# Optimization experiments

Hardware: AMD Instinct MI355X
Metric: run time of the kernel (lower is better)

Reference implementation:

```python
import jax, jax.numpy as jnp
import numpy as np

N = 100000   # nodes
E = 1600000  # edges (avg degree 16)
D = 64       # in_dim == hidden_dim
L = 3        # num_layers
EPS = 1e-5   # LayerNorm eps


def setup_inputs() -> dict:
    key = jax.random.key(0)
    k0, k1, k2 = jax.random.split(key, 3)
    x = jax.random.normal(k0, (N, D), dtype=jnp.float32)
    edge_index = jax.random.randint(k1, (2, E), 0, N, dtype=jnp.int32)
    # Per-layer GCN weights/bias (Glorot-ish scale) and LayerNorm params
    Ws = jax.random.normal(k2, (L, D, D), dtype=jnp.float32) / np.float32(np.sqrt(D))
    bs = jnp.zeros((L, D), dtype=jnp.float32)
    gammas = jnp.ones((L, D), dtype=jnp.float32)
    betas = jnp.zeros((L, D), dtype=jnp.float32)
    return {"x": x, "Ws": Ws, "bs": bs, "gammas": gammas, "betas": betas,
            "edge_index": edge_index}


def _layer_norm(h, gamma, beta):
    mu = jnp.mean(h, axis=-1, keepdims=True)
    var = jnp.mean(jnp.square(h - mu), axis=-1, keepdims=True)
    return (h - mu) * jax.lax.rsqrt(var + EPS) * gamma + beta


def reference(x, Ws, bs, gammas, betas, edge_index):
    # GCNConv semantics: add self-loops, symmetric deg^{-1/2} normalization.
    loop = jnp.arange(N, dtype=edge_index.dtype)
    row = jnp.concatenate([edge_index[0], loop])  # source (gather)
    col = jnp.concatenate([edge_index[1], loop])  # target (scatter)
    deg = jax.ops.segment_sum(jnp.ones_like(col, dtype=x.dtype), col, num_segments=N)
    dinv = jnp.where(deg > 0, jax.lax.rsqrt(deg), jnp.zeros_like(deg))
    enorm = dinv[row] * dinv[col]  # (E+N,)

    h = x
    for i in range(L):
        hw = h @ Ws[i]                                   # (N, D) small GEMM
        msg = hw[row] * enorm[:, None]                   # (E+N, D) gather
        h = jax.ops.segment_sum(msg, col, num_segments=N) + bs[i]  # scatter-add
        h = _layer_norm(h, gammas[i], betas[i])
        if i < L - 1:
            h = jax.nn.relu(h)                           # dropout is identity in eval
    return h
```

## Files before the change

### kernel.cpp

```cpp
#include <hip/hip_runtime.h>
#include <hip/hip_bf16.h>


#define DDIM 64
#define EPSV 1e-5f
#define BSHIFT 9
#define BNODES (1 << BSHIFT)
#define NBUCK 256
#define CHUNK 4096

typedef __hip_bfloat16 bf16;
typedef unsigned int u32;
typedef unsigned short u16;
typedef unsigned long long u64;
typedef __attribute__((ext_vector_type(8))) short frag8;
typedef __attribute__((ext_vector_type(4))) float f32x4;

__device__ __forceinline__ float b2f(bf16 v) { return __bfloat162float(v); }
__device__ __forceinline__ float bits2f(u16 b) {
    union { u32 u; float f; } c; c.u = ((u32)b) << 16; return c.f;
}
__device__ __forceinline__ float lo2f(u32 u) {
    union { u32 x; float f; } c; c.x = u << 16; return c.f;
}
__device__ __forceinline__ float hi2f(u32 u) {
    union { u32 x; float f; } c; c.x = u & 0xffff0000u; return c.f;
}
__device__ __forceinline__ u32 packbf(float a, float b) {
    union { bf16 h; u16 u; } ca, cb;
    ca.h = __float2bfloat16(a);
    cb.h = __float2bfloat16(b);
    return (u32)ca.u | ((u32)cb.u << 16);
}
__device__ __forceinline__ float cvt_load(const void* src, int i, int f32) {
    return f32 ? ((const float*)src)[i] : b2f(((const bf16*)src)[i]);
}

__global__ void detect_dtype(const u32* __restrict__ g, int* __restrict__ flagF32) {
    if (threadIdx.x == 0 && blockIdx.x == 0) *flagF32 = (g[0] == 0x3F800000u) ? 1 : 0;
}

__global__ void convert_x(const void* __restrict__ src, bf16* __restrict__ dst,
                          const int* __restrict__ flagF32,
                          const float* __restrict__ dinv, int n) {
    int i = blockIdx.x * blockDim.x + threadIdx.x;
    if (i >= n) return;
    dst[i] = __float2bfloat16(cvt_load(src, i, *flagF32) * dinv[i >> 6]);
}

__global__ void convert_params(const void* __restrict__ W, const void* __restrict__ b,
                               const void* __restrict__ g, const void* __restrict__ bt,
                               bf16* __restrict__ dWt, bf16* __restrict__ db,
                               bf16* __restrict__ dg, bf16* __restrict__ dbt,
                               const int* __restrict__ flagF32, int nW, int nS) {
    int i = blockIdx.x * blockDim.x + threadIdx.x;
    int f = *flagF32;
    if (i < nW) {
        int L = i >> 12, n = (i >> 6) & 63, k = i & 63;
        dWt[i] = __float2bfloat16(cvt_load(W, (L << 12) | (k << 6) | n, f));
        return;
    }
    i -= nW;
    if (i < nS) { db[i] = __float2bfloat16(cvt_load(b, i, f)); return; }
    i -= nS;
    if (i < nS) { dg[i] = __float2bfloat16(cvt_load(g, i, f)); return; }
    i -= nS;
    if (i < nS) { dbt[i] = __float2bfloat16(cvt_load(bt, i, f)); }
}


__global__ void __launch_bounds__(256) bucket_count(const int* __restrict__ col,
                                                    int* __restrict__ bcnt, int E) {
    __shared__ int h[NBUCK];
    int tid = threadIdx.x;
    h[tid] = 0;
    __syncthreads();
    for (int i = blockIdx.x * blockDim.x + tid; i < E; i += gridDim.x * blockDim.x)
        atomicAdd(&h[col[i] >> BSHIFT], 1);
    __syncthreads();
    int v = h[tid];
    if (v) atomicAdd(&bcnt[tid], v);
}

__global__ void bucket_scan(const int* __restrict__ bcnt, int* __restrict__ bbase,
                            int* __restrict__ gcur, int nbuck, int E) {
    __shared__ int s[NBUCK];
    int tid = threadIdx.x;
    int v = (tid < nbuck) ? bcnt[tid] : 0;
    s[tid] = v;
    __syncthreads();
    for (int off = 1; off < NBUCK; off <<= 1) {
        int t = (tid >= off) ? s[tid - off] : 0;
        __syncthreads();
        s[tid] += t;
        __syncthreads();
    }
    int excl = s[tid] - v;
    if (tid < nbuck) { bbase[tid] = excl; gcur[tid] = excl; }
    if (tid == 0) bbase[nbuck] = E;
}

__global__ void __launch_bounds__(256) partition_edges(const int* __restrict__ row,
                                                       const int* __restrict__ col,
                                                       int* __restrict__ gcur,
                                                       u64* __restrict__ pairs, int E) {
    __shared__ int hist[NBUCK];
    __shared__ int lbase[NBUCK];
    __shared__ int gdelta[NBUCK];
    __shared__ int lcur[NBUCK];
    __shared__ int sbuf[NBUCK];
    __shared__ int dest[CHUNK];
    __shared__ u64 stage[CHUNK];
    int tid = threadIdx.x;
    int chunk0 = blockIdx.x * CHUNK;
    hist[tid] = 0;
    lcur[tid] = 0;
    __syncthreads();
    int r[16], c[16];
#pragma unroll
    for (int i = 0; i < 16; i++) {
        int idx = chunk0 + i * 256 + tid;
        if (idx < E) {
            r[i] = row[idx];
            c[i] = col[idx];
            atomicAdd(&hist[c[i] >> BSHIFT], 1);
        }
    }
    __syncthreads();
    int h = hist[tid];
    sbuf[tid] = h;
    __syncthreads();
    for (int off = 1; off < 256; off <<= 1) {
        int t = (tid >= off) ? sbuf[tid - off] : 0;
        __syncthreads();
        sbuf[tid] += t;
        __syncthreads();
    }
    int excl = sbuf[tid] - h;
    lbase[tid] = excl;
    int gb = (h > 0) ? atomicAdd(&gcur[tid], h) : 0;
    gdelta[tid] = gb - excl;
    __syncthreads();
#pragma unroll
    for (int i = 0; i < 16; i++) {
        int idx = chunk0 + i * 256 + tid;
        if (idx < E) {
            int b = c[i] >> BSHIFT;
            int pos = lbase[b] + atomicAdd(&lcur[b], 1);
            stage[pos] = ((u64)(u32)c[i] << 32) | (u32)r[i];
            dest[pos] = gdelta[b];
        }
    }
    __syncthreads();
    int chunkN = min(CHUNK, E - chunk0);
    for (int j = tid; j < chunkN; j += 256)
        pairs[(size_t)(dest[j] + j)] = stage[j];
}

__global__ void __launch_bounds__(512) build_csr(const u64* __restrict__ pairs,
                                                 const int* __restrict__ bbase,
                                                 int* __restrict__ ptr,
                                                 int* __restrict__ srcs,
                                                 float* __restrict__ dinv,
                                                 int N, int E) {
    __shared__ int deg[BNODES];
    __shared__ int lptr[BNODES];
    __shared__ int lfill[BNODES];
    int b = blockIdx.x;
    int node0 = b << BSHIFT;
    int nn = min(BNODES, N - node0);
    int tid = threadIdx.x;
    deg[tid] = 0;
    lfill[tid] = 0;
    __syncthreads();
    int beg = bbase[b], end = bbase[b + 1];
    for (int i = beg + tid; i < end; i += 512)
        atomicAdd(&deg[(int)(pairs[i] >> 32) - node0], 1);
    __syncthreads();
    int d = deg[tid];
    lptr[tid] = d;
    __syncthreads();
    for (int off = 1; off < BNODES; off <<= 1) {
        int t = (tid >= off) ? lptr[tid - off] : 0;
        __syncthreads();
        lptr[tid] += t;
        __syncthreads();
    }
    int excl = lptr[tid] - d;
    lptr[tid] = beg + excl;
    if (tid < nn) {
        ptr[node0 + tid] = beg + excl;
        dinv[node0 + tid] = rsqrtf((float)(d + 1));
    }
    if (b == 0 && tid == 0) ptr[N] = E;
    __syncthreads();
    for (int i = beg + tid; i < end; i += 512) {
        u64 pr = pairs[i];
        int li = (int)(pr >> 32) - node0;
        int p = lptr[li] + atomicAdd(&lfill[li], 1);
        srcs[p] = (int)(pr & 0xffffffffu);
    }
}


__global__ void __launch_bounds__(256) aggregate(const bf16* __restrict__ Hs,
                                                 const int* __restrict__ ptr,
                                                 const int* __restrict__ srcs,
                                                 const float* __restrict__ dinv,
                                                 bf16* __restrict__ AG, int N) {
    int t = blockIdx.x * blockDim.x + threadIdx.x;
    int w = t >> 6;
    int lane = t & 63;
    int half = lane >> 5;
    int lane32 = lane & 31;
    int v = w * 2 + half;
    if (v >= N) return;
    int sub = lane32 >> 3;
    int quad = lane & 7;
    uint4 selfq = ((const uint4*)(Hs + ((size_t)v << 6)))[quad];
    int beg = ptr[v], end = ptr[v + 1];
    float a0 = 0.f, a1 = 0.f, a2 = 0.f, a3 = 0.f;
    float a4 = 0.f, a5 = 0.f, a6 = 0.f, a7 = 0.f;
    for (int base = beg; base < end; base += 32) {
        int rem = end - base;
        int m = rem < 32 ? rem : 32;
        int sidx = (lane32 < m) ? srcs[base + lane32] : 0;
        for (int j = 0; j < m; j += 8) {
            int e0 = j + sub;
            int e1 = j + 4 + sub;
            int s0 = __shfl(sidx, (half << 5) + e0, 64);
            int s1 = __shfl(sidx, (half << 5) + e1, 64);
            float k0 = (e0 < m) ? 1.f : 0.f;
            float k1 = (e1 < m) ? 1.f : 0.f;
            uint4 q0 = ((const uint4*)(Hs + ((size_t)s0 << 6)))[quad];
            uint4 q1 = ((const uint4*)(Hs + ((size_t)s1 << 6)))[quad];
            a0 = fmaf(lo2f(q0.x), k0, a0); a1 = fmaf(hi2f(q0.x), k0, a1);
            a2 = fmaf(lo2f(q0.y), k0, a2); a3 = fmaf(hi2f(q0.y), k0, a3);
            a4 = fmaf(lo2f(q0.z), k0, a4); a5 = fmaf(hi2f(q0.z), k0, a5);
            a6 = fmaf(lo2f(q0.w), k0, a6); a7 = fmaf(hi2f(q0.w), k0, a7);
            a0 = fmaf(lo2f(q1.x), k1, a0); a1 = fmaf(hi2f(q1.x), k1, a1);
            a2 = fmaf(lo2f(q1.y), k1, a2); a3 = fmaf(hi2f(q1.y), k1, a3);
            a4 = fmaf(lo2f(q1.z), k1, a4); a5 = fmaf(hi2f(q1.z), k1, a5);
            a6 = fmaf(lo2f(q1.w), k1, a6); a7 = fmaf(hi2f(q1.w), k1, a7);
        }
    }
#pragma unroll
    for (int d = 8; d < 32; d <<= 1) {
        a0 += __shfl_xor(a0, d, 64); a1 += __shfl_xor(a1, d, 64);
        a2 += __shfl_xor(a2, d, 64); a3 += __shfl_xor(a3, d, 64);
        a4 += __shfl_xor(a4, d, 64); a5 += __shfl_xor(a5, d, 64);
        a6 += __shfl_xor(a6, d, 64); a7 += __shfl_xor(a7, d, 64);
    }
    if (sub == 0) {
        a0 += lo2f(selfq.x); a1 += hi2f(selfq.x);
        a2 += lo2f(selfq.y); a3 += hi2f(selfq.y);
        a4 += lo2f(selfq.z); a5 += hi2f(selfq.z);
        a6 += lo2f(selfq.w); a7 += hi2f(selfq.w);
        float dv = dinv[v];
        uint4 o;
        o.x = packbf(a0 * dv, a1 * dv);
        o.y = packbf(a2 * dv, a3 * dv);
        o.z = packbf(a4 * dv, a5 * dv);
        o.w = packbf(a6 * dv, a7 * dv);
        ((uint4*)(AG + ((size_t)v << 6)))[quad] = o;
    }
}


__global__ void __launch_bounds__(256, 4) gemm_ln(const bf16* __restrict__ AG,
                                                  const bf16* __restrict__ Wt,
                                                  const bf16* __restrict__ bias,
                                                  const bf16* __restrict__ gamma,
                                                  const bf16* __restrict__ beta,
                                                  bf16* __restrict__ outB,
                                                  float* __restrict__ outF,
                                                  const int* __restrict__ flagF32,
                                                  const float* __restrict__ dscale,
                                                  int relu, int last, int N) {
    int tid = threadIdx.x;
    int wv = tid >> 6, lane = tid & 63;
    int n = lane & 15, q = lane >> 4;
    int r0 = blockIdx.x * 64 + wv * 16;

    int arow = r0 + n;
    int arowc = arow < N ? arow : N - 1;
    const uint4* ap = (const uint4*)(AG + ((size_t)arowc << 6));
    frag8 af0 = __builtin_bit_cast(frag8, ap[q]);
    frag8 af1 = __builtin_bit_cast(frag8, ap[4 + q]);

    f32x4 acc[4];
#pragma unroll
    for (int t = 0; t < 4; t++) acc[t] = (f32x4){0.f, 0.f, 0.f, 0.f};
#pragma unroll
    for (int t = 0; t < 4; t++) {
        const uint4* bp = (const uint4*)(Wt + (((size_t)(t * 16 + n)) << 6));
        frag8 bf0 = __builtin_bit_cast(frag8, bp[q]);
        frag8 bf1 = __builtin_bit_cast(frag8, bp[4 + q]);
        acc[t] = __builtin_amdgcn_mfma_f32_16x16x32_bf16(af0, bf0, acc[t], 0, 0, 0);
        acc[t] = __builtin_amdgcn_mfma_f32_16x16x32_bf16(af1, bf1, acc[t], 0, 0, 0);
    }

    float bb[4], gg[4], be[4];
#pragma unroll
    for (int t = 0; t < 4; t++) {
        int c = t * 16 + n;
        bb[t] = b2f(bias[c]);
        gg[t] = b2f(gamma[c]);
        be[t] = b2f(beta[c]);
    }
    int f32o = last ? flagF32[0] : 0;

#pragma unroll
    for (int r = 0; r < 4; r++) {
        int rr = r0 + q * 4 + r;
        float v0 = acc[0][r] + bb[0];
        float v1 = acc[1][r] + bb[1];
        float v2 = acc[2][r] + bb[2];
        float v3 = acc[3][r] + bb[3];
        float s = v0 + v1 + v2 + v3;
        s += __shfl_xor(s, 1, 64);
        s += __shfl_xor(s, 2, 64);
        s += __shfl_xor(s, 4, 64);
        s += __shfl_xor(s, 8, 64);
        float mu = s * (1.f / 64.f);
        float d0 = v0 - mu, d1 = v1 - mu, d2 = v2 - mu, d3 = v3 - mu;
        float sq = d0 * d0 + d1 * d1 + d2 * d2 + d3 * d3;
        sq += __shfl_xor(sq, 1, 64);
        sq += __shfl_xor(sq, 2, 64);
        sq += __shfl_xor(sq, 4, 64);
        sq += __shfl_xor(sq, 8, 64);
        float rs = rsqrtf(sq * (1.f / 64.f) + EPSV);
        float o0 = d0 * rs * gg[0] + be[0];
        float o1 = d1 * rs * gg[1] + be[1];
        float o2 = d2 * rs * gg[2] + be[2];
        float o3 = d3 * rs * gg[3] + be[3];
        if (relu) {
            o0 = fmaxf(o0, 0.f); o1 = fmaxf(o1, 0.f);
            o2 = fmaxf(o2, 0.f); o3 = fmaxf(o3, 0.f);
        }
        if (rr < N) {
            if (dscale) {
                float sc = dscale[rr];
                o0 *= sc; o1 *= sc; o2 *= sc; o3 *= sc;
            }
            size_t base = ((size_t)rr << 6) + n;
            if (f32o) {
                outF[base] = o0; outF[base + 16] = o1;
                outF[base + 32] = o2; outF[base + 48] = o3;
            } else {
                outB[base] = __float2bfloat16(o0);
                outB[base + 16] = __float2bfloat16(o1);
                outB[base + 32] = __float2bfloat16(o2);
                outB[base + 48] = __float2bfloat16(o3);
            }
        }
    }
}


extern "C" void kernel_launch(void* const* d_in, const int* in_sizes, int n_in,
                              void* d_out, int out_size, void* d_ws, size_t ws_size,
                              hipStream_t stream) {
    (void)n_in; (void)out_size; (void)ws_size;
    const void* x      = d_in[0];
    const void* Wsrc   = d_in[1];
    const void* bsrc   = d_in[2];
    const void* gsrc   = d_in[3];
    const void* btsrc  = d_in[4];
    const int*  ei     = (const int*)d_in[5];
    int N = in_sizes[0] / DDIM;
    int E = in_sizes[5] / 2;
    const int* rowp = ei;
    const int* colp = ei + E;

    char* w = (char*)d_ws;
    auto alloc = [&](size_t bytes) -> char* {
        char* p = w;
        w += (bytes + 255) / 256 * 256;
        return p;
    };
    int*   flag  = (int*)alloc(4);
    int*   gcur  = (int*)alloc(NBUCK * 4);
    int*   bcnt  = (int*)alloc(NBUCK * 4);
    int*   bbase = (int*)alloc((NBUCK + 1) * 4);
    int*   ptr   = (int*)alloc((size_t)(N + 1) * 4);
    int*   srcs  = (int*)alloc((size_t)E * 4);
    float* dinv  = (float*)alloc((size_t)N * 4);
    char*  hreg  = alloc((size_t)N * DDIM * 2);
    bf16*  H     = (bf16*)hreg;
    u64*   pairs = (u64*)hreg;
    bf16*  wsW   = (bf16*)alloc((size_t)3 * 4096 * 2);
    bf16*  wsB   = (bf16*)alloc(192 * 2);
    bf16*  wsG   = (bf16*)alloc(192 * 2);
    bf16*  wsBt  = (bf16*)alloc(192 * 2);
    bf16*  AG    = (bf16*)alloc((size_t)N * DDIM * 2);

    const int tb = 256;
    int nbuck = (N + BNODES - 1) >> BSHIFT;
    detect_dtype<<<1, 64, 0, stream>>>((const u32*)gsrc, flag);
    hipMemsetAsync(bcnt, 0, NBUCK * 4, stream);
    bucket_count<<<256, tb, 0, stream>>>(colp, bcnt, E);
    bucket_scan<<<1, NBUCK, 0, stream>>>(bcnt, bbase, gcur, nbuck, E);
    partition_edges<<<(E + CHUNK - 1) / CHUNK, tb, 0, stream>>>(rowp, colp, gcur, pairs, E);
    build_csr<<<nbuck, 512, 0, stream>>>(pairs, bbase, ptr, srcs, dinv, N, E);

    convert_x<<<(N * DDIM + tb - 1) / tb, tb, 0, stream>>>(x, H, flag, dinv, N * DDIM);
    int nPar = 3 * 4096 + 3 * 192;
    convert_params<<<(nPar + tb - 1) / tb, tb, 0, stream>>>(Wsrc, bsrc, gsrc, btsrc,
                                                            wsW, wsB, wsG, wsBt,
                                                            flag, 3 * 4096, 192);

    int aggBlocks = (N * 32 + tb - 1) / tb;
    int gBlocks = (N + 63) / 64;

    aggregate<<<aggBlocks, tb, 0, stream>>>(H, ptr, srcs, dinv, AG, N);
    gemm_ln<<<gBlocks, tb, 0, stream>>>(AG, wsW + 0 * 4096, wsB + 0,   wsG + 0,   wsBt + 0,
                                        H, nullptr, flag, dinv, 1, 0, N);
    aggregate<<<aggBlocks, tb, 0, stream>>>(H, ptr, srcs, dinv, AG, N);
    gemm_ln<<<gBlocks, tb, 0, stream>>>(AG, wsW + 1 * 4096, wsB + 64,  wsG + 64,  wsBt + 64,
                                        H, nullptr, flag, dinv, 1, 0, N);
    aggregate<<<aggBlocks, tb, 0, stream>>>(H, ptr, srcs, dinv, AG, N);
    gemm_ln<<<gBlocks, tb, 0, stream>>>(AG, wsW + 2 * 4096, wsB + 128, wsG + 128, wsBt + 128,
                                        (bf16*)d_out, (float*)d_out, flag, nullptr, 0, 1, N);
}
```

Before: 290.9 us.

## Fuse aggregation with GEMM+LayerNorm and merge setup kernels

Merges the per-layer aggregate kernel into the GEMM+LayerNorm kernel. Each wave aggregates its 16 rows into LDS, then feeds the MFMA directly, which removes the intermediate AG round-trip through global memory and one launch per layer. H is now ping-ponged between two buffers because the layer output can no longer overwrite its input. The setup also drops kernels: dtype detection moves into bucket_count, per-block partial histograms replace global atomics and the memset, and the x and parameter conversions become one kernel. The cost is less gather parallelism per wave (8 serial iterations per wave), which may expose gather latency under the raised occupancy hint.

```diff
diff --git a/kernel.cpp b/kernel.cpp
--- a/kernel.cpp
+++ b/kernel.cpp
@@ -8,6 +8,7 @@
 #define BNODES (1 << BSHIFT)
 #define NBUCK 256
 #define CHUNK 4096
+#define CBLKS 256
 
 typedef __hip_bfloat16 bf16;
 typedef unsigned int u32;
@@ -17,9 +18,6 @@
 typedef __attribute__((ext_vector_type(4))) float f32x4;
 
 __device__ __forceinline__ float b2f(bf16 v) { return __bfloat162float(v); }
-__device__ __forceinline__ float bits2f(u16 b) {
-    union { u32 u; float f; } c; c.u = ((u32)b) << 16; return c.f;
-}
 __device__ __forceinline__ float lo2f(u32 u) {
     union { u32 x; float f; } c; c.x = u << 16; return c.f;
 }
@@ -36,57 +34,28 @@
     return f32 ? ((const float*)src)[i] : b2f(((const bf16*)src)[i]);
 }
 
-__global__ void detect_dtype(const u32* __restrict__ g, int* __restrict__ flagF32) {
-    if (threadIdx.x == 0 && blockIdx.x == 0) *flagF32 = (g[0] == 0x3F800000u) ? 1 : 0;
-}
-
-__global__ void convert_x(const void* __restrict__ src, bf16* __restrict__ dst,
-                          const int* __restrict__ flagF32,
-                          const float* __restrict__ dinv, int n) {
-    int i = blockIdx.x * blockDim.x + threadIdx.x;
-    if (i >= n) return;
-    dst[i] = __float2bfloat16(cvt_load(src, i, *flagF32) * dinv[i >> 6]);
-}
-
-__global__ void convert_params(const void* __restrict__ W, const void* __restrict__ b,
-                               const void* __restrict__ g, const void* __restrict__ bt,
-                               bf16* __restrict__ dWt, bf16* __restrict__ db,
-                               bf16* __restrict__ dg, bf16* __restrict__ dbt,
-                               const int* __restrict__ flagF32, int nW, int nS) {
-    int i = blockIdx.x * blockDim.x + threadIdx.x;
-    int f = *flagF32;
-    if (i < nW) {
-        int L = i >> 12, n = (i >> 6) & 63, k = i & 63;
-        dWt[i] = __float2bfloat16(cvt_load(W, (L << 12) | (k << 6) | n, f));
-        return;
-    }
-    i -= nW;
-    if (i < nS) { db[i] = __float2bfloat16(cvt_load(b, i, f)); return; }
-    i -= nS;
-    if (i < nS) { dg[i] = __float2bfloat16(cvt_load(g, i, f)); return; }
-    i -= nS;
-    if (i < nS) { dbt[i] = __float2bfloat16(cvt_load(bt, i, f)); }
-}
-
 
 __global__ void __launch_bounds__(256) bucket_count(const int* __restrict__ col,
-                                                    int* __restrict__ bcnt, int E) {
+                                                    int* __restrict__ partials,
+                                                    const u32* __restrict__ g,
+                                                    int* __restrict__ flagF32, int E) {
     __shared__ int h[NBUCK];
     int tid = threadIdx.x;
+    if (blockIdx.x == 0 && tid == 0) *flagF32 = (g[0] == 0x3F800000u) ? 1 : 0;
     h[tid] = 0;
     __syncthreads();
     for (int i = blockIdx.x * blockDim.x + tid; i < E; i += gridDim.x * blockDim.x)
         atomicAdd(&h[col[i] >> BSHIFT], 1);
     __syncthreads();
-    int v = h[tid];
-    if (v) atomicAdd(&bcnt[tid], v);
-}
-
-__global__ void bucket_scan(const int* __restrict__ bcnt, int* __restrict__ bbase,
+    partials[blockIdx.x * NBUCK + tid] = h[tid];
+}
+
+__global__ void bucket_scan(const int* __restrict__ partials, int* __restrict__ bbase,
                             int* __restrict__ gcur, int nbuck, int E) {
     __shared__ int s[NBUCK];
     int tid = threadIdx.x;
-    int v = (tid < nbuck) ? bcnt[tid] : 0;
+    int v = 0;
+    for (int b = 0; b < CBLKS; b++) v += partials[b * NBUCK + tid];
     s[tid] = v;
     __syncthreads();
     for (int off = 1; off < NBUCK; off <<= 1) {
@@ -202,91 +171,108 @@
     }
 }
 
-
-__global__ void __launch_bounds__(256) aggregate(const bf16* __restrict__ Hs,
-                                                 const int* __restrict__ ptr,
-                                                 const int* __restrict__ srcs,
-                                                 const float* __restrict__ dinv,
-                                                 bf16* __restrict__ AG, int N) {
-    int t = blockIdx.x * blockDim.x + threadIdx.x;
-    int w = t >> 6;
-    int lane = t & 63;
-    int half = lane >> 5;
-    int lane32 = lane & 31;
-    int v = w * 2 + half;
-    if (v >= N) return;
-    int sub = lane32 >> 3;
-    int quad = lane & 7;
-    uint4 selfq = ((const uint4*)(Hs + ((size_t)v << 6)))[quad];
-    int beg = ptr[v], end = ptr[v + 1];
-    float a0 = 0.f, a1 = 0.f, a2 = 0.f, a3 = 0.f;
-    float a4 = 0.f, a5 = 0.f, a6 = 0.f, a7 = 0.f;
-    for (int base = beg; base < end; base += 32) {
-        int rem = end - base;
-        int m = rem < 32 ? rem : 32;
-        int sidx = (lane32 < m) ? srcs[base + lane32] : 0;
-        for (int j = 0; j < m; j += 8) {
-            int e0 = j + sub;
-            int e1 = j + 4 + sub;
-            int s0 = __shfl(sidx, (half << 5) + e0, 64);
-            int s1 = __shfl(sidx, (half << 5) + e1, 64);
-            float k0 = (e0 < m) ? 1.f : 0.f;
-            float k1 = (e1 < m) ? 1.f : 0.f;
-            uint4 q0 = ((const uint4*)(Hs + ((size_t)s0 << 6)))[quad];
-            uint4 q1 = ((const uint4*)(Hs + ((size_t)s1 << 6)))[quad];
-            a0 = fmaf(lo2f(q0.x), k0, a0); a1 = fmaf(hi2f(q0.x), k0, a1);
-            a2 = fmaf(lo2f(q0.y), k0, a2); a3 = fmaf(hi2f(q0.y), k0, a3);
-            a4 = fmaf(lo2f(q0.z), k0, a4); a5 = fmaf(hi2f(q0.z), k0, a5);
-            a6 = fmaf(lo2f(q0.w), k0, a6); a7 = fmaf(hi2f(q0.w), k0, a7);
-            a0 = fmaf(lo2f(q1.x), k1, a0); a1 = fmaf(hi2f(q1.x), k1, a1);
-            a2 = fmaf(lo2f(q1.y), k1, a2); a3 = fmaf(hi2f(q1.y), k1, a3);
-            a4 = fmaf(lo2f(q1.z), k1, a4); a5 = fmaf(hi2f(q1.z), k1, a5);
-            a6 = fmaf(lo2f(q1.w), k1, a6); a7 = fmaf(hi2f(q1.w), k1, a7);
-        }
-    }
-#pragma unroll
-    for (int d = 8; d < 32; d <<= 1) {
-        a0 += __shfl_xor(a0, d, 64); a1 += __shfl_xor(a1, d, 64);
-        a2 += __shfl_xor(a2, d, 64); a3 += __shfl_xor(a3, d, 64);
-        a4 += __shfl_xor(a4, d, 64); a5 += __shfl_xor(a5, d, 64);
-        a6 += __shfl_xor(a6, d, 64); a7 += __shfl_xor(a7, d, 64);
-    }
-    if (sub == 0) {
-        a0 += lo2f(selfq.x); a1 += hi2f(selfq.x);
-        a2 += lo2f(selfq.y); a3 += hi2f(selfq.y);
-        a4 += lo2f(selfq.z); a5 += hi2f(selfq.z);
-        a6 += lo2f(selfq.w); a7 += hi2f(selfq.w);
-        float dv = dinv[v];
-        uint4 o;
-        o.x = packbf(a0 * dv, a1 * dv);
-        o.y = packbf(a2 * dv, a3 * dv);
-        o.z = packbf(a4 * dv, a5 * dv);
-        o.w = packbf(a6 * dv, a7 * dv);
-        ((uint4*)(AG + ((size_t)v << 6)))[quad] = o;
-    }
-}
-
-
-__global__ void __launch_bounds__(256, 4) gemm_ln(const bf16* __restrict__ AG,
-                                                  const bf16* __restrict__ Wt,
-                                                  const bf16* __restrict__ bias,
-                                                  const bf16* __restrict__ gamma,
-                                                  const bf16* __restrict__ beta,
-                                                  bf16* __restrict__ outB,
-                                                  float* __restrict__ outF,
-                                                  const int* __restrict__ flagF32,
-                                                  const float* __restrict__ dscale,
-                                                  int relu, int last, int N) {
+__global__ void convert_all(const void* __restrict__ x, const void* __restrict__ W,
+                            const void* __restrict__ b, const void* __restrict__ g,
+                            const void* __restrict__ bt,
+                            bf16* __restrict__ H, bf16* __restrict__ dWt,
+                            bf16* __restrict__ db, bf16* __restrict__ dg,
+                            bf16* __restrict__ dbt,
+                            const int* __restrict__ flagF32,
+                            const float* __restrict__ dinv, int nX, int nW, int nS) {
+    int i = blockIdx.x * blockDim.x + threadIdx.x;
+    int f = *flagF32;
+    if (i < nX) { H[i] = __float2bfloat16(cvt_load(x, i, f) * dinv[i >> 6]); return; }
+    i -= nX;
+    if (i < nW) {
+        int L = i >> 12, n = (i >> 6) & 63, k = i & 63;
+        dWt[i] = __float2bfloat16(cvt_load(W, (L << 12) | (k << 6) | n, f));
+        return;
+    }
+    i -= nW;
+    if (i < nS) { db[i] = __float2bfloat16(cvt_load(b, i, f)); return; }
+    i -= nS;
+    if (i < nS) { dg[i] = __float2bfloat16(cvt_load(g, i, f)); return; }
+    i -= nS;
+    if (i < nS) { dbt[i] = __float2bfloat16(cvt_load(bt, i, f)); }
+}
+
+
+__global__ void __launch_bounds__(256, 5) fused_layer(const bf16* __restrict__ Hs,
+                                                      const int* __restrict__ ptr,
+                                                      const int* __restrict__ srcs,
+                                                      const float* __restrict__ dinv,
+                                                      const bf16* __restrict__ Wt,
+                                                      const bf16* __restrict__ bias,
+                                                      const bf16* __restrict__ gamma,
+                                                      const bf16* __restrict__ beta,
+                                                      bf16* __restrict__ outB,
+                                                      float* __restrict__ outF,
+                                                      const int* __restrict__ flagF32,
+                                                      const float* __restrict__ dscale,
+                                                      int relu, int last, int N) {
+    __shared__ __align__(16) bf16 lsA[4][16][64];
     int tid = threadIdx.x;
     int wv = tid >> 6, lane = tid & 63;
+    int half = lane >> 5, lane32 = lane & 31;
+    int sub = lane32 >> 3, quad = lane & 7;
+    int r0 = blockIdx.x * 64 + wv * 16;
+
+    for (int it = 0; it < 8; it++) {
+        int v = r0 + it * 2 + half;
+        int vc = v < N ? v : N - 1;
+        uint4 selfq = ((const uint4*)(Hs + ((size_t)vc << 6)))[quad];
+        int beg = 0, end = 0;
+        if (v < N) { beg = ptr[v]; end = ptr[v + 1]; }
+        float a0 = 0.f, a1 = 0.f, a2 = 0.f, a3 = 0.f;
+        float a4 = 0.f, a5 = 0.f, a6 = 0.f, a7 = 0.f;
+        for (int base = beg; base < end; base += 32) {
+            int rem = end - base;
+            int m = rem < 32 ? rem : 32;
+            int sidx = (lane32 < m) ? srcs[base + lane32] : 0;
+            for (int j = 0; j < m; j += 8) {
+                int e0 = j + sub;
+                int e1 = j + 4 + sub;
+                int s0 = __shfl(sidx, (half << 5) + e0, 64);
+                int s1 = __shfl(sidx, (half << 5) + e1, 64);
+                float k0 = (e0 < m) ? 1.f : 0.f;
+                float k1 = (e1 < m) ? 1.f : 0.f;
+                uint4 q0 = ((const uint4*)(Hs + ((size_t)s0 << 6)))[quad];
+                uint4 q1 = ((const uint4*)(Hs + ((size_t)s1 << 6)))[quad];
+                a0 = fmaf(lo2f(q0.x), k0, a0); a1 = fmaf(hi2f(q0.x), k0, a1);
+                a2 = fmaf(lo2f(q0.y), k0, a2); a3 = fmaf(hi2f(q0.y), k0, a3);
+                a4 = fmaf(lo2f(q0.z), k0, a4); a5 = fmaf(hi2f(q0.z), k0, a5);
+                a6 = fmaf(lo2f(q0.w), k0, a6); a7 = fmaf(hi2f(q0.w), k0, a7);
+                a0 = fmaf(lo2f(q1.x), k1, a0); a1 = fmaf(hi2f(q1.x), k1, a1);
+                a2 = fmaf(lo2f(q1.y), k1, a2); a3 = fmaf(hi2f(q1.y), k1, a3);
+                a4 = fmaf(lo2f(q1.z), k1, a4); a5 = fmaf(hi2f(q1.z), k1, a5);
+                a6 = fmaf(lo2f(q1.w), k1, a6); a7 = fmaf(hi2f(q1.w), k1, a7);
+            }
+        }
+#pragma unroll
+        for (int d = 8; d < 32; d <<= 1) {
+            a0 += __shfl_xor(a0, d, 64); a1 += __shfl_xor(a1, d, 64);
+            a2 += __shfl_xor(a2, d, 64); a3 += __shfl_xor(a3, d, 64);
+            a4 += __shfl_xor(a4, d, 64); a5 += __shfl_xor(a5, d, 64);
+            a6 += __shfl_xor(a6, d, 64); a7 += __shfl_xor(a7, d, 64);
+        }
+        if (sub == 0 && v < N) {
+            a0 += lo2f(selfq.x); a1 += hi2f(selfq.x);
+            a2 += lo2f(selfq.y); a3 += hi2f(selfq.y);
+            a4 += lo2f(selfq.z); a5 += hi2f(selfq.z);
+            a6 += lo2f(selfq.w); a7 += hi2f(selfq.w);
+            float dv = dinv[v];
+            uint4 o;
+            o.x = packbf(a0 * dv, a1 * dv);
+            o.y = packbf(a2 * dv, a3 * dv);
+            o.z = packbf(a4 * dv, a5 * dv);
+            o.w = packbf(a6 * dv, a7 * dv);
+            *(uint4*)&lsA[wv][it * 2 + half][quad * 8] = o;
+        }
+    }
+
     int n = lane & 15, q = lane >> 4;
-    int r0 = blockIdx.x * 64 + wv * 16;
-
-    int arow = r0 + n;
-    int arowc = arow < N ? arow : N - 1;
-    const uint4* ap = (const uint4*)(AG + ((size_t)arowc << 6));
-    frag8 af0 = __builtin_bit_cast(frag8, ap[q]);
-    frag8 af1 = __builtin_bit_cast(frag8, ap[4 + q]);
+    frag8 af0 = *(const frag8*)&lsA[wv][n][q * 8];
+    frag8 af1 = *(const frag8*)&lsA[wv][n][32 + q * 8];
 
     f32x4 acc[4];
 #pragma unroll
@@ -381,7 +367,7 @@
     };
     int*   flag  = (int*)alloc(4);
     int*   gcur  = (int*)alloc(NBUCK * 4);
-    int*   bcnt  = (int*)alloc(NBUCK * 4);
+    int*   parts = (int*)alloc((size_t)CBLKS * NBUCK * 4);
     int*   bbase = (int*)alloc((NBUCK + 1) * 4);
     int*   ptr   = (int*)alloc((size_t)(N + 1) * 4);
     int*   srcs  = (int*)alloc((size_t)E * 4);
@@ -393,33 +379,29 @@
     bf16*  wsB   = (bf16*)alloc(192 * 2);
     bf16*  wsG   = (bf16*)alloc(192 * 2);
     bf16*  wsBt  = (bf16*)alloc(192 * 2);
-    bf16*  AG    = (bf16*)alloc((size_t)N * DDIM * 2);
+    bf16*  H2    = (bf16*)alloc((size_t)N * DDIM * 2);
 
     const int tb = 256;
     int nbuck = (N + BNODES - 1) >> BSHIFT;
-    detect_dtype<<<1, 64, 0, stream>>>((const u32*)gsrc, flag);
-    hipMemsetAsync(bcnt, 0, NBUCK * 4, stream);
-    bucket_count<<<256, tb, 0, stream>>>(colp, bcnt, E);
-    bucket_scan<<<1, NBUCK, 0, stream>>>(bcnt, bbase, gcur, nbuck, E);
+    bucket_count<<<CBLKS, tb, 0, stream>>>(colp, parts, (const u32*)gsrc, flag, E);
+    bucket_scan<<<1, NBUCK, 0, stream>>>(parts, bbase, gcur, nbuck, E);
     partition_edges<<<(E + CHUNK - 1) / CHUNK, tb, 0, stream>>>(rowp, colp, gcur, pairs, E);
     build_csr<<<nbuck, 512, 0, stream>>>(pairs, bbase, ptr, srcs, dinv, N, E);
 
-    convert_x<<<(N * DDIM + tb - 1) / tb, tb, 0, stream>>>(x, H, flag, dinv, N * DDIM);
-    int nPar = 3 * 4096 + 3 * 192;
-    convert_params<<<(nPar + tb - 1) / tb, tb, 0, stream>>>(Wsrc, bsrc, gsrc, btsrc,
-                                                            wsW, wsB, wsG, wsBt,
-                                                            flag, 3 * 4096, 192);
-
-    int aggBlocks = (N * 32 + tb - 1) / tb;
+    int nX = N * DDIM, nW = 3 * 4096, nS = 192;
+    int nAll = nX + nW + 3 * nS;
+    convert_all<<<(nAll + tb - 1) / tb, tb, 0, stream>>>(x, Wsrc, bsrc, gsrc, btsrc,
+                                                         H, wsW, wsB, wsG, wsBt,
+                                                         flag, dinv, nX, nW, nS);
+
     int gBlocks = (N + 63) / 64;
-
-    aggregate<<<aggBlocks, tb, 0, stream>>>(H, ptr, srcs, dinv, AG, N);
-    gemm_ln<<<gBlocks, tb, 0, stream>>>(AG, wsW + 0 * 4096, wsB + 0,   wsG + 0,   wsBt + 0,
-                                        H, nullptr, flag, dinv, 1, 0, N);
-    aggregate<<<aggBlocks, tb, 0, stream>>>(H, ptr, srcs, dinv, AG, N);
-    gemm_ln<<<gBlocks, tb, 0, stream>>>(AG, wsW + 1 * 4096, wsB + 64,  wsG + 64,  wsBt + 64,
-                                        H, nullptr, flag, dinv, 1, 0, N);
-    aggregate<<<aggBlocks, tb, 0, stream>>>(H, ptr, srcs, dinv, AG, N);
-    gemm_ln<<<gBlocks, tb, 0, stream>>>(AG, wsW + 2 * 4096, wsB + 128, wsG + 128, wsBt + 128,
-                                        (bf16*)d_out, (float*)d_out, flag, nullptr, 0, 1, N);
-}
+    fused_layer<<<gBlocks, tb, 0, stream>>>(H, ptr, srcs, dinv,
+                                            wsW + 0 * 4096, wsB + 0,   wsG + 0,   wsBt + 0,
+                                            H2, nullptr, flag, dinv, 1, 0, N);
+    fused_layer<<<gBlocks, tb, 0, stream>>>(H2, ptr, srcs, dinv,
+                                            wsW + 1 * 4096, wsB + 64,  wsG + 64,  wsBt + 64,
+                                            H, nullptr, flag, dinv, 1, 0, N);
+    fused_layer<<<gBlocks, tb, 0, stream>>>(H, ptr, srcs, dinv,
+                                            wsW + 2 * 4096, wsB + 128, wsG + 128, wsBt + 128,
+                                            (bf16*)d_out, (float*)d_out, flag, nullptr, 0, 1, N);
+}
```

Result: faster. 256.0 us (-12.0%).
